# Optimization experiments

Measured on AMD Instinct MI355X. Metric: run time of the kernel, lower is better.

Reference implementation:

```python
import jax, jax.numpy as jnp
import numpy as np

WX, WY = 32, 32
N = WX * WY                      # 1024 tokens
TOKEN_DIM = 1024
QKV = 512
H = 8
HD = QKV // H                    # 64
TOPK = 32
B = 64
NUM_UNIQUE = (2 * WX - 1) * (2 * WY - 1)  # 3969 unique relative offsets
LN_EPS = 1e-5


def _make_rel_idx():
    # identical to torch create_positional_biases: lexicographic unique index of (dx, dy)
    ix = np.arange(N) // WY
    iy = np.arange(N) % WY
    dx = ix[:, None] - ix[None, :]
    dy = iy[:, None] - iy[None, :]
    rel = (dx + WX - 1) * (2 * WY - 1) + (dy + WY - 1)
    return jnp.asarray(rel, dtype=jnp.int32)  # [N, N]


def _layernorm(x, g, b):
    m = jnp.mean(x, axis=-1, keepdims=True)
    v = jnp.mean(jnp.square(x - m), axis=-1, keepdims=True)
    return (x - m) * jax.lax.rsqrt(v + LN_EPS) * g + b


def setup_inputs() -> dict:
    key = jax.random.key(0)
    ks = jax.random.split(key, 12)
    s = 0.02
    return {
        "x": jax.random.normal(ks[0], (B, N, TOKEN_DIM), jnp.float32),
        "scorer_w": jax.random.normal(ks[1], (1, TOKEN_DIM), jnp.float32) * s,
        "scorer_b": jnp.zeros((1,), jnp.float32),
        "ln_g": jnp.ones((TOKEN_DIM,), jnp.float32),
        "ln_b": jnp.zeros((TOKEN_DIM,), jnp.float32),
        "qk_w": jax.random.normal(ks[2], (QKV, TOKEN_DIM), jnp.float32) * s,
        "qk_b": jnp.zeros((QKV,), jnp.float32),
        "v_w": jax.random.normal(ks[3], (QKV, TOKEN_DIM), jnp.float32) * s,
        "v_b": jnp.zeros((QKV,), jnp.float32),
        "skip_w": jax.random.normal(ks[4], (QKV, TOKEN_DIM), jnp.float32) * s,
        "skip_b": jnp.zeros((QKV,), jnp.float32),
        "out_w": jax.random.normal(ks[5], (QKV, QKV), jnp.float32) * s,
        "out_b": jnp.zeros((QKV,), jnp.float32),
        "fc_w": jax.random.normal(ks[6], (2, QKV), jnp.float32) * s,
        "fc_b": jnp.zeros((2,), jnp.float32),
        "unique_bias": jax.random.normal(ks[7], (NUM_UNIQUE,), jnp.float32) * s,
        "rel_idx": _make_rel_idx(),
    }


def reference(x, scorer_w, scorer_b, ln_g, ln_b, qk_w, qk_b, v_w, v_b,
              skip_w, skip_b, out_w, out_b, fc_w, fc_b, unique_bias, rel_idx):
    # token selection (eval path: argmax of relevance logits)
    logits = jnp.einsum('bnd,od->bno', x, scorer_w)[..., 0] + scorer_b[0]  # [B, N]
    sel_idx = jnp.argmax(logits, axis=-1)                                   # [B]
    sel_tok = x[jnp.arange(B), sel_idx]                                     # [B, D]

    x_n = _layernorm(x, ln_g, ln_b)
    s_n = _layernorm(sel_tok, ln_g, ln_b)

    value = (jnp.einsum('bnd,qd->bnq', x_n, v_w) + v_b).reshape(B, N, H, HD).transpose(0, 2, 1, 3)  # [B,H,N,hd]
    key_t = (jnp.einsum('bnd,qd->bnq', x_n, qk_w) + qk_b).reshape(B, N, H, HD).transpose(0, 2, 1, 3)
    query = (s_n @ qk_w.T + qk_b).reshape(B, H, HD)                         # [B,H,hd]

    attn = jnp.einsum('bhd,bhnd->bhn', query, key_t) / jnp.sqrt(jnp.float32(HD))  # [B,H,N]
    bias = unique_bias[rel_idx[sel_idx]]                                    # gather: [B, N]
    attn = jax.nn.softmax(attn + bias[:, None, :], axis=-1)

    # top-k sparsification + renormalization
    _, topk_idx = jax.lax.top_k(attn, TOPK)                                 # [B,H,K]
    mask = jax.nn.one_hot(topk_idx, N, dtype=attn.dtype).sum(axis=-2)       # [B,H,N] 0/1
    attn = attn * mask
    attn = attn / (attn.sum(axis=-1, keepdims=True) + 1e-9)

    y = jnp.einsum('bhn,bhnd->bhd', attn, value).reshape(B, QKV)            # [B, QKV]
    skip = sel_tok @ skip_w.T + skip_b
    y = jax.nn.relu(y + skip)
    # dropout is identity in eval mode
    y = y @ out_w.T + out_b
    y = y @ fc_w.T + fc_b
    return y  # [B, 2]
```

## Files before the change

### kernel.cpp

```cpp
#include <hip/hip_runtime.h>
#include <hip/hip_bf16.h>
#include <math.h>

#define WX 32
#define WY 32
#define NTOK 1024
#define TD 1024
#define QKV 512
#define NH 8
#define HD 64
#define TOPK 32
#define BB 64

__device__ __forceinline__ float wred_sum(float v){
  #pragma unroll
  for (int o=32;o;o>>=1) v += __shfl_xor(v,o,64);
  return v;
}
__device__ __forceinline__ float wred_max(float v){
  #pragma unroll
  for (int o=32;o;o>>=1) v = fmaxf(v, __shfl_xor(v,o,64));
  return v;
}
__device__ __forceinline__ float dot4f(float4 a, float4 b){
  return a.x*b.x + a.y*b.y + a.z*b.z + a.w*b.w;
}

__global__ __launch_bounds__(256) void k1_stats(
    const float* __restrict__ x, const float* __restrict__ sw, const float* __restrict__ sb,
    float* __restrict__ mean, float* __restrict__ rstd, float* __restrict__ logit){
  int wave = threadIdx.x >> 6, lane = threadIdx.x & 63;
  int tok = blockIdx.x*4 + wave;
  const float4* xp = (const float4*)(x + (size_t)tok*TD);
  const float4* sp = (const float4*)sw;
  float s1=0.f, s2=0.f, sd=0.f;
  #pragma unroll
  for (int j=0;j<4;j++){
    float4 v = xp[lane + j*64];
    float4 w = sp[lane + j*64];
    s1 += v.x+v.y+v.z+v.w;
    s2 += v.x*v.x + v.y*v.y + v.z*v.z + v.w*v.w;
    sd += dot4f(v,w);
  }
  s1 = wred_sum(s1); s2 = wred_sum(s2); sd = wred_sum(sd);
  if (lane==0){
    float m = s1*(1.f/1024.f);
    float var = s2*(1.f/1024.f) - m*m;
    mean[tok] = m;
    rstd[tok] = rsqrtf(var + 1e-5f);
    logit[tok] = sd + sb[0];
  }
}

__global__ __launch_bounds__(256) void k2_prep(
    const float* __restrict__ x, const float* __restrict__ logit,
    const float* __restrict__ mean, const float* __restrict__ rstd,
    const float* __restrict__ lng, const float* __restrict__ lnb,
    const float* __restrict__ qkw, const float* __restrict__ qkb,
    int* __restrict__ selI, float* __restrict__ gu8,
    float* __restrict__ Aw, float* __restrict__ C0w){
  __shared__ float sn[TD];
  __shared__ float qs[QKV];
  __shared__ float redV[4]; __shared__ int redI[4];
  __shared__ float red16[64];
  __shared__ int sel_s;
  int b = blockIdx.x, t = threadIdx.x, lane = t&63, wave = t>>6;

  const float* lg = logit + b*NTOK;
  float bv = -INFINITY; int bi = 0;
  #pragma unroll
  for (int j=0;j<4;j++){ int idx = t*4+j; float v = lg[idx]; if (v > bv){ bv=v; bi=idx; } }
  #pragma unroll
  for (int o=32;o;o>>=1){
    float vv = __shfl_xor(bv,o,64); int ii = __shfl_xor(bi,o,64);
    if (vv > bv || (vv == bv && ii < bi)){ bv=vv; bi=ii; }
  }
  if (lane==0){ redV[wave]=bv; redI[wave]=bi; }
  __syncthreads();
  if (t==0){
    float v = redV[0]; int i = redI[0];
    for (int w=1; w<4; w++){ if (redV[w] > v || (redV[w]==v && redI[w]<i)){ v=redV[w]; i=redI[w]; } }
    sel_s = i; selI[b] = i;
  }
  __syncthreads();
  int sel = sel_s;
  float m = mean[b*NTOK+sel], r = rstd[b*NTOK+sel];
  float4 g4 = ((const float4*)lng)[t];
  float4 b4 = ((const float4*)lnb)[t];
  {
    float4 xv = ((const float4*)(x + ((size_t)b*NTOK + sel)*TD))[t];
    float4 s4;
    s4.x = (xv.x-m)*r*g4.x + b4.x;
    s4.y = (xv.y-m)*r*g4.y + b4.y;
    s4.z = (xv.z-m)*r*g4.z + b4.z;
    s4.w = (xv.w-m)*r*g4.w + b4.w;
    ((float4*)sn)[t] = s4;
  }
  __syncthreads();
  #pragma unroll
  for (int rr=0; rr<2; rr++){
    int j = t + rr*256;
    const float4* wr = (const float4*)(qkw + (size_t)j*TD);
    float acc = 0.f;
    for (int d=0; d<256; d++) acc += dot4f(wr[d], ((const float4*)sn)[d]);
    qs[j] = acc + qkb[j];
  }
  __syncthreads();
  float su[NH], bu[NH];
  #pragma unroll
  for (int h=0; h<NH; h++){
    float4 acc = make_float4(0.f,0.f,0.f,0.f);
    for (int c=0; c<HD; c++){
      float qv = qs[h*HD+c];
      float4 w = ((const float4*)(qkw + (size_t)(h*HD+c)*TD))[t];
      acc.x += qv*w.x; acc.y += qv*w.y; acc.z += qv*w.z; acc.w += qv*w.w;
    }
    su[h] = g4.x*acc.x + g4.y*acc.y + g4.z*acc.z + g4.w*acc.w;
    bu[h] = b4.x*acc.x + b4.y*acc.y + b4.z*acc.z + b4.w*acc.w;
    float4 gu;
    gu.x = acc.x*g4.x*0.125f; gu.y = acc.y*g4.y*0.125f;
    gu.z = acc.z*g4.z*0.125f; gu.w = acc.w*g4.w*0.125f;
    ((float4*)(gu8 + ((size_t)b*NH + h)*TD))[t] = gu;
  }
  #pragma unroll
  for (int h=0; h<NH; h++){ su[h] = wred_sum(su[h]); bu[h] = wred_sum(bu[h]); }
  if (lane==0){
    #pragma unroll
    for (int h=0; h<NH; h++){ red16[wave*16+h] = su[h]; red16[wave*16+8+h] = bu[h]; }
  }
  __syncthreads();
  if (t < NH){
    int h = t;
    float s = 0.f, bb = 0.f;
    for (int w=0; w<4; w++){ s += red16[w*16+h]; bb += red16[w*16+8+h]; }
    float qb = 0.f;
    for (int c=0; c<HD; c++) qb += qs[h*HD+c]*qkb[h*HD+c];
    Aw[b*NH+h] = s*0.125f;
    C0w[b*NH+h] = (bb + qb)*0.125f;
  }
}

__global__ __launch_bounds__(128) void k3_attn(
    const float* __restrict__ x, const float* __restrict__ mean, const float* __restrict__ rstd,
    const float* __restrict__ gu8, const float* __restrict__ Aw, const float* __restrict__ C0w,
    const int* __restrict__ selI, const int* __restrict__ relIdx, const float* __restrict__ ub,
    float* __restrict__ attL){
  int b = blockIdx.x >> 3;
  int n = (blockIdx.x & 7)*128 + threadIdx.x;
  int tok = b*NTOK + n;
  float m = mean[tok], r = rstd[tok];
  int sel = selI[b];
  float bias = ub[relIdx[sel*NTOK + n]];
  const float4* xp = (const float4*)(x + (size_t)tok*TD);
  const float4* gp = (const float4*)(gu8 + (size_t)b*NH*TD);
  float4 acc[NH];
  #pragma unroll
  for (int h=0; h<NH; h++) acc[h] = make_float4(0.f,0.f,0.f,0.f);
  for (int d0=0; d0<256; d0+=4){
    #pragma unroll
    for (int jj=0; jj<4; jj++){
      float4 xv = xp[d0+jj];
      #pragma unroll
      for (int h=0; h<NH; h++){
        float4 g = gp[h*256 + d0 + jj];
        acc[h].x += xv.x*g.x; acc[h].y += xv.y*g.y;
        acc[h].z += xv.z*g.z; acc[h].w += xv.w*g.w;
      }
    }
  }
  #pragma unroll
  for (int h=0; h<NH; h++){
    float s = acc[h].x + acc[h].y + acc[h].z + acc[h].w;
    float L = r*s - r*m*Aw[b*NH+h] + C0w[b*NH+h] + bias;
    attL[((size_t)b*NH + h)*NTOK + n] = L;
  }
}

__global__ __launch_bounds__(256) void k4_topkv(
    const float* __restrict__ x, const float* __restrict__ mean, const float* __restrict__ rstd,
    const float* __restrict__ lng, const float* __restrict__ lnb,
    const float* __restrict__ vw, const float* __restrict__ vb,
    const float* __restrict__ attL, float* __restrict__ yout){
  __shared__ float candV[4]; __shared__ int candI[4];
  __shared__ float redf[4];
  __shared__ float selV[TOPK]; __shared__ int selIs[TOPK];
  __shared__ float aa[TOPK]; __shared__ float am[TOPK];
  __shared__ float xbar[TD];
  __shared__ float red2[256];
  int b = blockIdx.x >> 3, h = blockIdx.x & 7;
  int t = threadIdx.x, lane = t&63, wave = t>>6;

  float4 Lv = ((const float4*)(attL + ((size_t)b*NH + h)*NTOK))[t];
  float lm = fmaxf(fmaxf(Lv.x,Lv.y), fmaxf(Lv.z,Lv.w));
  lm = wred_max(lm);
  if (lane==0) redf[wave] = lm;
  __syncthreads();
  float maxL = fmaxf(fmaxf(redf[0],redf[1]), fmaxf(redf[2],redf[3]));
  __syncthreads();
  float ev[4];
  ev[0] = __expf(Lv.x - maxL); ev[1] = __expf(Lv.y - maxL);
  ev[2] = __expf(Lv.z - maxL); ev[3] = __expf(Lv.w - maxL);
  float zp = ev[0]+ev[1]+ev[2]+ev[3];
  zp = wred_sum(zp);
  if (lane==0) redf[wave] = zp;
  __syncthreads();
  float Z = redf[0]+redf[1]+redf[2]+redf[3];
  __syncthreads();

  float S = 0.f;
  for (int k=0; k<TOPK; k++){
    float bv = -1.f; int bi = 1<<20;
    #pragma unroll
    for (int j=0;j<4;j++){ if (ev[j] > bv){ bv = ev[j]; bi = t*4+j; } }
    #pragma unroll
    for (int o=32;o;o>>=1){
      float vv = __shfl_xor(bv,o,64); int ii = __shfl_xor(bi,o,64);
      if (vv > bv || (vv == bv && ii < bi)){ bv=vv; bi=ii; }
    }
    if (lane==0){ candV[wave]=bv; candI[wave]=bi; }
    __syncthreads();
    float wv = candV[0]; int wi = candI[0];
    #pragma unroll
    for (int w=1; w<4; w++){
      float vv = candV[w]; int ii = candI[w];
      if (vv > wv || (vv == wv && ii < wi)){ wv=vv; wi=ii; }
    }
    if ((wi>>2) == t) ev[wi&3] = -1.f;
    if (t==0){ selV[k]=wv; selIs[k]=wi; }
    S += wv;
    __syncthreads();
  }

  float denom = S + 1e-9f*Z;
  float W = S/denom;
  if (t < TOPK){
    int ni = selIs[t];
    float w = selV[t]/denom;
    float a = w * rstd[b*NTOK+ni];
    aa[t] = a; am[t] = a*mean[b*NTOK+ni];
  }
  __syncthreads();
  float c = 0.f;
  #pragma unroll
  for (int k=0;k<TOPK;k++) c += am[k];

  float4 acc = make_float4(0.f,0.f,0.f,0.f);
  for (int k=0;k<TOPK;k++){
    float a = aa[k];
    float4 xv = ((const float4*)(x + ((size_t)b*NTOK + selIs[k])*TD))[t];
    acc.x += a*xv.x; acc.y += a*xv.y; acc.z += a*xv.z; acc.w += a*xv.w;
  }
  float4 g4 = ((const float4*)lng)[t];
  float4 b4 = ((const float4*)lnb)[t];
  float4 xb;
  xb.x = g4.x*(acc.x - c) + b4.x*W;
  xb.y = g4.y*(acc.y - c) + b4.y*W;
  xb.z = g4.z*(acc.z - c) + b4.z*W;
  xb.w = g4.w*(acc.w - c) + b4.w*W;
  ((float4*)xbar)[t] = xb;
  __syncthreads();

  int co = t >> 2, part = t & 3;
  const float4* vp = (const float4*)(vw + (size_t)(h*HD+co)*TD + part*256);
  const float4* xp2 = ((const float4*)xbar) + part*64;
  float a2 = 0.f;
  for (int j=0;j<64;j++) a2 += dot4f(vp[j], xp2[j]);
  red2[t] = a2;
  __syncthreads();
  if (part==0){
    float y = red2[t] + red2[t+1] + red2[t+2] + red2[t+3] + vb[h*HD+co]*W;
    yout[b*QKV + h*HD + co] = y;
  }
}

__global__ __launch_bounds__(256) void k5_epi(
    const float* __restrict__ x, const int* __restrict__ selI,
    const float* __restrict__ skw, const float* __restrict__ skb,
    const float* __restrict__ ow, const float* __restrict__ ob,
    const float* __restrict__ fcw, const float* __restrict__ fcb,
    const float* __restrict__ yv, float* __restrict__ out){
  __shared__ float xs[TD];
  __shared__ float t1[QKV];
  __shared__ float t2[QKV];
  __shared__ float redA[4]; __shared__ float redB[4];
  int b = blockIdx.x, t = threadIdx.x, lane = t&63, wave = t>>6;
  int sel = selI[b];
  ((float4*)xs)[t] = ((const float4*)(x + ((size_t)b*NTOK + sel)*TD))[t];
  __syncthreads();
  #pragma unroll
  for (int rr=0; rr<2; rr++){
    int j = t + rr*256;
    const float4* wr = (const float4*)(skw + (size_t)j*TD);
    float acc = 0.f;
    for (int d=0; d<256; d++) acc += dot4f(wr[d], ((const float4*)xs)[d]);
    t1[j] = fmaxf(yv[b*QKV + j] + acc + skb[j], 0.f);
  }
  __syncthreads();
  #pragma unroll
  for (int rr=0; rr<2; rr++){
    int j = t + rr*256;
    const float4* wr = (const float4*)(ow + (size_t)j*QKV);
    float acc = 0.f;
    for (int d=0; d<128; d++) acc += dot4f(wr[d], ((const float4*)t1)[d]);
    t2[j] = acc + ob[j];
  }
  __syncthreads();
  float a0 = 0.f, a1 = 0.f;
  #pragma unroll
  for (int rr=0; rr<2; rr++){
    int d = t + rr*256;
    float v = t2[d];
    a0 += v*fcw[d]; a1 += v*fcw[QKV+d];
  }
  a0 = wred_sum(a0); a1 = wred_sum(a1);
  if (lane==0){ redA[wave]=a0; redB[wave]=a1; }
  __syncthreads();
  if (t==0){
    out[b*2+0] = redA[0]+redA[1]+redA[2]+redA[3] + fcb[0];
    out[b*2+1] = redB[0]+redB[1]+redB[2]+redB[3] + fcb[1];
  }
}

extern "C" void kernel_launch(void* const* d_in, const int* in_sizes, int n_in,
                              void* d_out, int out_size, void* d_ws, size_t ws_size,
                              hipStream_t stream) {
  const float* x   = (const float*)d_in[0];
  const float* sw  = (const float*)d_in[1];
  const float* sb  = (const float*)d_in[2];
  const float* lng = (const float*)d_in[3];
  const float* lnb = (const float*)d_in[4];
  const float* qkw = (const float*)d_in[5];
  const float* qkb = (const float*)d_in[6];
  const float* vw  = (const float*)d_in[7];
  const float* vb  = (const float*)d_in[8];
  const float* skw = (const float*)d_in[9];
  const float* skb = (const float*)d_in[10];
  const float* ow  = (const float*)d_in[11];
  const float* ob  = (const float*)d_in[12];
  const float* fcw = (const float*)d_in[13];
  const float* fcb = (const float*)d_in[14];
  const float* ub  = (const float*)d_in[15];
  const int*   ri  = (const int*)d_in[16];
  float* out = (float*)d_out;

  float* wsf   = (float*)d_ws;
  float* logit = wsf;
  float* mean  = wsf + 65536;
  float* rstd  = wsf + 131072;
  int*   selI  = (int*)(wsf + 196608);
  float* gu8   = wsf + 196672;
  float* Aw    = wsf + 720960;
  float* C0w   = wsf + 721472;
  float* attL  = wsf + 721984;
  float* yv    = wsf + 1246272;

  k1_stats<<<16384, 256, 0, stream>>>(x, sw, sb, mean, rstd, logit);
  k2_prep<<<BB, 256, 0, stream>>>(x, logit, mean, rstd, lng, lnb, qkw, qkb,
                                  selI, gu8, Aw, C0w);
  k3_attn<<<BB*8, 128, 0, stream>>>(x, mean, rstd, gu8, Aw, C0w, selI, ri, ub, attL);
  k4_topkv<<<BB*NH, 256, 0, stream>>>(x, mean, rstd, lng, lnb, vw, vb, attL, yv);
  k5_epi<<<BB, 256, 0, stream>>>(x, selI, skw, skb, ow, ob, fcw, fcb, yv, out);
}
```

Baseline: 680.9 us.

## Parallelize prep, attention, top-k and epilogue kernels across more blocks

Splits the per-batch prep kernel across heads (B*H blocks) and precomputes the relative-position bias once per batch. Rewrites the attention-logit kernel so each wave handles a token, with gu vectors held in registers, coalesced x loads with prefetch, and wave reductions. Replaces the serial block-wide top-k with per-wave top-32 lists merged by one thread, and splits the epilogue into three wider-grid kernels with split-K dot products. This targets underutilized low-block-count kernels and uncoalesced per-thread x row reads, at the cost of redundant argmax/layernorm work per head and extra launches.

```diff
diff --git a/kernel.cpp b/kernel.cpp
--- a/kernel.cpp
+++ b/kernel.cpp
@@ -57,14 +57,16 @@
     const float* __restrict__ mean, const float* __restrict__ rstd,
     const float* __restrict__ lng, const float* __restrict__ lnb,
     const float* __restrict__ qkw, const float* __restrict__ qkb,
+    const int* __restrict__ relIdx, const float* __restrict__ ub,
     int* __restrict__ selI, float* __restrict__ gu8,
-    float* __restrict__ Aw, float* __restrict__ C0w){
+    float* __restrict__ Aw, float* __restrict__ C0w, float* __restrict__ biasArr){
   __shared__ float sn[TD];
-  __shared__ float qs[QKV];
+  __shared__ float qs[HD];
+  __shared__ float red[256];
   __shared__ float redV[4]; __shared__ int redI[4];
-  __shared__ float red16[64];
   __shared__ int sel_s;
-  int b = blockIdx.x, t = threadIdx.x, lane = t&63, wave = t>>6;
+  int b = blockIdx.x >> 3, h = blockIdx.x & 7;
+  int t = threadIdx.x, lane = t&63, wave = t>>6;
 
   const float* lg = logit + b*NTOK;
   float bv = -INFINITY; int bi = 0;
@@ -80,7 +82,8 @@
   if (t==0){
     float v = redV[0]; int i = redI[0];
     for (int w=1; w<4; w++){ if (redV[w] > v || (redV[w]==v && redI[w]<i)){ v=redV[w]; i=redI[w]; } }
-    sel_s = i; selI[b] = i;
+    sel_s = i;
+    if (h==0) selI[b] = i;
   }
   __syncthreads();
   int sel = sel_s;
@@ -97,82 +100,108 @@
     ((float4*)sn)[t] = s4;
   }
   __syncthreads();
-  #pragma unroll
-  for (int rr=0; rr<2; rr++){
-    int j = t + rr*256;
-    const float4* wr = (const float4*)(qkw + (size_t)j*TD);
+  {
+    int row = t>>2, part = t&3;
+    const float4* wr = (const float4*)(qkw + (size_t)(h*HD+row)*TD + part*256);
+    const float4* xp = ((const float4*)sn) + part*64;
     float acc = 0.f;
-    for (int d=0; d<256; d++) acc += dot4f(wr[d], ((const float4*)sn)[d]);
-    qs[j] = acc + qkb[j];
-  }
-  __syncthreads();
-  float su[NH], bu[NH];
-  #pragma unroll
-  for (int h=0; h<NH; h++){
-    float4 acc = make_float4(0.f,0.f,0.f,0.f);
-    for (int c=0; c<HD; c++){
-      float qv = qs[h*HD+c];
-      float4 w = ((const float4*)(qkw + (size_t)(h*HD+c)*TD))[t];
-      acc.x += qv*w.x; acc.y += qv*w.y; acc.z += qv*w.z; acc.w += qv*w.w;
-    }
-    su[h] = g4.x*acc.x + g4.y*acc.y + g4.z*acc.z + g4.w*acc.w;
-    bu[h] = b4.x*acc.x + b4.y*acc.y + b4.z*acc.z + b4.w*acc.w;
+    #pragma unroll 8
+    for (int j=0;j<64;j++) acc += dot4f(wr[j], xp[j]);
+    red[t] = acc;
+  }
+  __syncthreads();
+  if (t < HD) qs[t] = red[t*4]+red[t*4+1]+red[t*4+2]+red[t*4+3] + qkb[h*HD+t];
+  __syncthreads();
+  float4 acc = make_float4(0.f,0.f,0.f,0.f);
+  for (int c=0;c<HD;c++){
+    float qv = qs[c];
+    float4 w = ((const float4*)(qkw + (size_t)(h*HD+c)*TD))[t];
+    acc.x += qv*w.x; acc.y += qv*w.y; acc.z += qv*w.z; acc.w += qv*w.w;
+  }
+  {
     float4 gu;
     gu.x = acc.x*g4.x*0.125f; gu.y = acc.y*g4.y*0.125f;
     gu.z = acc.z*g4.z*0.125f; gu.w = acc.w*g4.w*0.125f;
-    ((float4*)(gu8 + ((size_t)b*NH + h)*TD))[t] = gu;
-  }
-  #pragma unroll
-  for (int h=0; h<NH; h++){ su[h] = wred_sum(su[h]); bu[h] = wred_sum(bu[h]); }
-  if (lane==0){
-    #pragma unroll
-    for (int h=0; h<NH; h++){ red16[wave*16+h] = su[h]; red16[wave*16+8+h] = bu[h]; }
-  }
-  __syncthreads();
-  if (t < NH){
-    int h = t;
-    float s = 0.f, bb = 0.f;
-    for (int w=0; w<4; w++){ s += red16[w*16+h]; bb += red16[w*16+8+h]; }
-    float qb = 0.f;
-    for (int c=0; c<HD; c++) qb += qs[h*HD+c]*qkb[h*HD+c];
-    Aw[b*NH+h] = s*0.125f;
-    C0w[b*NH+h] = (bb + qb)*0.125f;
-  }
-}
-
-__global__ __launch_bounds__(128) void k3_attn(
+    ((float4*)(gu8 + ((size_t)(b*NH+h))*TD))[t] = gu;
+  }
+  float su_p = g4.x*acc.x + g4.y*acc.y + g4.z*acc.z + g4.w*acc.w;
+  float bu_p = b4.x*acc.x + b4.y*acc.y + b4.z*acc.z + b4.w*acc.w;
+  su_p = wred_sum(su_p); bu_p = wred_sum(bu_p);
+  if (lane==0){ red[wave] = su_p; red[8+wave] = bu_p; }
+  if (wave==0){
+    float qb_p = qs[lane]*qkb[h*HD+lane];
+    qb_p = wred_sum(qb_p);
+    if (lane==0) red[16] = qb_p;
+  }
+  __syncthreads();
+  if (t==0){
+    float s  = red[0]+red[1]+red[2]+red[3];
+    float bb = red[8]+red[9]+red[10]+red[11];
+    Aw[b*NH+h]  = s*0.125f;
+    C0w[b*NH+h] = (bb + red[16])*0.125f;
+  }
+  if (h==0){
+    const int* rp = relIdx + (size_t)sel*NTOK;
+    #pragma unroll
+    for (int j=0;j<4;j++){
+      int n = t*4+j;
+      biasArr[b*NTOK+n] = ub[rp[n]];
+    }
+  }
+}
+
+__global__ __launch_bounds__(256) void k3_attn(
     const float* __restrict__ x, const float* __restrict__ mean, const float* __restrict__ rstd,
     const float* __restrict__ gu8, const float* __restrict__ Aw, const float* __restrict__ C0w,
-    const int* __restrict__ selI, const int* __restrict__ relIdx, const float* __restrict__ ub,
-    float* __restrict__ attL){
-  int b = blockIdx.x >> 3;
-  int n = (blockIdx.x & 7)*128 + threadIdx.x;
-  int tok = b*NTOK + n;
-  float m = mean[tok], r = rstd[tok];
-  int sel = selI[b];
-  float bias = ub[relIdx[sel*NTOK + n]];
-  const float4* xp = (const float4*)(x + (size_t)tok*TD);
+    const float* __restrict__ biasArr, float* __restrict__ attL){
+  int b = blockIdx.x >> 4;
+  int chunk = blockIdx.x & 15;
+  int lane = threadIdx.x & 63, wave = threadIdx.x >> 6;
+
   const float4* gp = (const float4*)(gu8 + (size_t)b*NH*TD);
-  float4 acc[NH];
-  #pragma unroll
-  for (int h=0; h<NH; h++) acc[h] = make_float4(0.f,0.f,0.f,0.f);
-  for (int d0=0; d0<256; d0+=4){
-    #pragma unroll
-    for (int jj=0; jj<4; jj++){
-      float4 xv = xp[d0+jj];
+  float4 G[NH][4];
+  #pragma unroll
+  for (int h=0;h<NH;h++)
+    #pragma unroll
+    for (int j=0;j<4;j++)
+      G[h][j] = gp[h*256 + j*64 + lane];
+  float Ah[NH], Ch[NH];
+  #pragma unroll
+  for (int h=0;h<NH;h++){ Ah[h] = Aw[b*NH+h]; Ch[h] = C0w[b*NH+h]; }
+
+  const int base = chunk*64 + wave*16;
+  float4 cur[4];
+  {
+    const float4* xp = (const float4*)(x + ((size_t)b*NTOK + base)*TD);
+    #pragma unroll
+    for (int j=0;j<4;j++) cur[j] = xp[j*64 + lane];
+  }
+  for (int i=0;i<16;i++){
+    int n = base + i;
+    int tok = b*NTOK + n;
+    float4 nxt[4];
+    if (i < 15){
+      const float4* xp = (const float4*)(x + (size_t)(tok+1)*TD);
       #pragma unroll
-      for (int h=0; h<NH; h++){
-        float4 g = gp[h*256 + d0 + jj];
-        acc[h].x += xv.x*g.x; acc[h].y += xv.y*g.y;
-        acc[h].z += xv.z*g.z; acc[h].w += xv.w*g.w;
-      }
-    }
-  }
-  #pragma unroll
-  for (int h=0; h<NH; h++){
-    float s = acc[h].x + acc[h].y + acc[h].z + acc[h].w;
-    float L = r*s - r*m*Aw[b*NH+h] + C0w[b*NH+h] + bias;
-    attL[((size_t)b*NH + h)*NTOK + n] = L;
+      for (int j=0;j<4;j++) nxt[j] = xp[j*64 + lane];
+    }
+    float m = mean[tok], r = rstd[tok], bias = biasArr[b*NTOK+n];
+    float s[NH];
+    #pragma unroll
+    for (int h=0;h<NH;h++){
+      float a = dot4f(cur[0],G[h][0]) + dot4f(cur[1],G[h][1])
+              + dot4f(cur[2],G[h][2]) + dot4f(cur[3],G[h][3]);
+      s[h] = wred_sum(a);
+    }
+    #pragma unroll
+    for (int h=0;h<NH;h++){
+      if (lane == h)
+        attL[((size_t)b*NH+h)*NTOK + n] = r*s[h] - r*m*Ah[h] + Ch[h] + bias;
+    }
+    if (i < 15){
+      #pragma unroll
+      for (int j=0;j<4;j++) cur[j] = nxt[j];
+    }
   }
 }
 
@@ -181,9 +210,10 @@
     const float* __restrict__ lng, const float* __restrict__ lnb,
     const float* __restrict__ vw, const float* __restrict__ vb,
     const float* __restrict__ attL, float* __restrict__ yout){
-  __shared__ float candV[4]; __shared__ int candI[4];
   __shared__ float redf[4];
+  __shared__ float wtopV[4][TOPK]; __shared__ int wtopI[4][TOPK];
   __shared__ float selV[TOPK]; __shared__ int selIs[TOPK];
+  __shared__ float Ssh;
   __shared__ float aa[TOPK]; __shared__ float am[TOPK];
   __shared__ float xbar[TD];
   __shared__ float red2[256];
@@ -205,10 +235,8 @@
   if (lane==0) redf[wave] = zp;
   __syncthreads();
   float Z = redf[0]+redf[1]+redf[2]+redf[3];
-  __syncthreads();
-
-  float S = 0.f;
-  for (int k=0; k<TOPK; k++){
+
+  for (int k=0;k<TOPK;k++){
     float bv = -1.f; int bi = 1<<20;
     #pragma unroll
     for (int j=0;j<4;j++){ if (ev[j] > bv){ bv = ev[j]; bi = t*4+j; } }
@@ -217,20 +245,31 @@
       float vv = __shfl_xor(bv,o,64); int ii = __shfl_xor(bi,o,64);
       if (vv > bv || (vv == bv && ii < bi)){ bv=vv; bi=ii; }
     }
-    if (lane==0){ candV[wave]=bv; candI[wave]=bi; }
-    __syncthreads();
-    float wv = candV[0]; int wi = candI[0];
-    #pragma unroll
-    for (int w=1; w<4; w++){
-      float vv = candV[w]; int ii = candI[w];
-      if (vv > wv || (vv == wv && ii < wi)){ wv=vv; wi=ii; }
-    }
-    if ((wi>>2) == t) ev[wi&3] = -1.f;
-    if (t==0){ selV[k]=wv; selIs[k]=wi; }
-    S += wv;
-    __syncthreads();
-  }
-
+    #pragma unroll
+    for (int j=0;j<4;j++){ if (bi == t*4+j) ev[j] = -1.f; }
+    if (lane==0){ wtopV[wave][k] = bv; wtopI[wave][k] = bi; }
+  }
+  __syncthreads();
+  if (t==0){
+    int p0=0,p1=0,p2=0,p3=0;
+    float S = 0.f;
+    for (int k=0;k<TOPK;k++){
+      float bv = -1.f; int bi = 1<<20, bw = 0;
+      float v; int ii;
+      v = wtopV[0][p0]; ii = wtopI[0][p0]; if (v > bv || (v==bv && ii<bi)){ bv=v; bi=ii; bw=0; }
+      v = wtopV[1][p1]; ii = wtopI[1][p1]; if (v > bv || (v==bv && ii<bi)){ bv=v; bi=ii; bw=1; }
+      v = wtopV[2][p2]; ii = wtopI[2][p2]; if (v > bv || (v==bv && ii<bi)){ bv=v; bi=ii; bw=2; }
+      v = wtopV[3][p3]; ii = wtopI[3][p3]; if (v > bv || (v==bv && ii<bi)){ bv=v; bi=ii; bw=3; }
+      if (bw==0) p0 = (p0<TOPK-1)?p0+1:p0;
+      else if (bw==1) p1 = (p1<TOPK-1)?p1+1:p1;
+      else if (bw==2) p2 = (p2<TOPK-1)?p2+1:p2;
+      else p3 = (p3<TOPK-1)?p3+1:p3;
+      selV[k] = bv; selIs[k] = bi; S += bv;
+    }
+    Ssh = S;
+  }
+  __syncthreads();
+  float S = Ssh;
   float denom = S + 1e-9f*Z;
   float W = S/denom;
   if (t < TOPK){
@@ -264,6 +303,7 @@
   const float4* vp = (const float4*)(vw + (size_t)(h*HD+co)*TD + part*256);
   const float4* xp2 = ((const float4*)xbar) + part*64;
   float a2 = 0.f;
+  #pragma unroll 8
   for (int j=0;j<64;j++) a2 += dot4f(vp[j], xp2[j]);
   red2[t] = a2;
   __syncthreads();
@@ -273,52 +313,65 @@
   }
 }
 
-__global__ __launch_bounds__(256) void k5_epi(
+__global__ __launch_bounds__(256) void k5a(
     const float* __restrict__ x, const int* __restrict__ selI,
     const float* __restrict__ skw, const float* __restrict__ skb,
-    const float* __restrict__ ow, const float* __restrict__ ob,
-    const float* __restrict__ fcw, const float* __restrict__ fcb,
-    const float* __restrict__ yv, float* __restrict__ out){
+    const float* __restrict__ yv, float* __restrict__ t1ws){
   __shared__ float xs[TD];
-  __shared__ float t1[QKV];
-  __shared__ float t2[QKV];
-  __shared__ float redA[4]; __shared__ float redB[4];
-  int b = blockIdx.x, t = threadIdx.x, lane = t&63, wave = t>>6;
+  __shared__ float red[256];
+  int b = blockIdx.x >> 3, chunk = blockIdx.x & 7;
+  int t = threadIdx.x;
   int sel = selI[b];
   ((float4*)xs)[t] = ((const float4*)(x + ((size_t)b*NTOK + sel)*TD))[t];
   __syncthreads();
-  #pragma unroll
-  for (int rr=0; rr<2; rr++){
-    int j = t + rr*256;
-    const float4* wr = (const float4*)(skw + (size_t)j*TD);
-    float acc = 0.f;
-    for (int d=0; d<256; d++) acc += dot4f(wr[d], ((const float4*)xs)[d]);
-    t1[j] = fmaxf(yv[b*QKV + j] + acc + skb[j], 0.f);
-  }
-  __syncthreads();
-  #pragma unroll
-  for (int rr=0; rr<2; rr++){
-    int j = t + rr*256;
-    const float4* wr = (const float4*)(ow + (size_t)j*QKV);
-    float acc = 0.f;
-    for (int d=0; d<128; d++) acc += dot4f(wr[d], ((const float4*)t1)[d]);
-    t2[j] = acc + ob[j];
-  }
-  __syncthreads();
+  int row = chunk*64 + (t>>2), part = t&3;
+  const float4* wr = (const float4*)(skw + (size_t)row*TD + part*256);
+  const float4* xp = ((const float4*)xs) + part*64;
+  float acc = 0.f;
+  #pragma unroll 8
+  for (int j=0;j<64;j++) acc += dot4f(wr[j], xp[j]);
+  red[t] = acc;
+  __syncthreads();
+  if (part==0){
+    float v = red[t]+red[t+1]+red[t+2]+red[t+3];
+    t1ws[b*QKV+row] = fmaxf(yv[b*QKV+row] + v + skb[row], 0.f);
+  }
+}
+
+__global__ __launch_bounds__(256) void k5b(
+    const float* __restrict__ t1ws, const float* __restrict__ ow,
+    const float* __restrict__ ob, float* __restrict__ t2ws){
+  __shared__ float ts[QKV];
+  __shared__ float red[256];
+  int b = blockIdx.x >> 3, chunk = blockIdx.x & 7;
+  int t = threadIdx.x;
+  if (t < 128) ((float4*)ts)[t] = ((const float4*)(t1ws + (size_t)b*QKV))[t];
+  __syncthreads();
+  int row = chunk*64 + (t>>2), part = t&3;
+  const float4* wr = (const float4*)(ow + (size_t)row*QKV + part*128);
+  const float4* xp = ((const float4*)ts) + part*32;
+  float acc = 0.f;
+  #pragma unroll
+  for (int j=0;j<32;j++) acc += dot4f(wr[j], xp[j]);
+  red[t] = acc;
+  __syncthreads();
+  if (part==0)
+    t2ws[b*QKV+row] = red[t]+red[t+1]+red[t+2]+red[t+3] + ob[row];
+}
+
+__global__ __launch_bounds__(64) void k5c(
+    const float* __restrict__ t2ws, const float* __restrict__ fcw,
+    const float* __restrict__ fcb, float* __restrict__ out){
+  int b = blockIdx.x, lane = threadIdx.x;
   float a0 = 0.f, a1 = 0.f;
   #pragma unroll
-  for (int rr=0; rr<2; rr++){
-    int d = t + rr*256;
-    float v = t2[d];
+  for (int j=0;j<8;j++){
+    int d = j*64 + lane;
+    float v = t2ws[(size_t)b*QKV + d];
     a0 += v*fcw[d]; a1 += v*fcw[QKV+d];
   }
   a0 = wred_sum(a0); a1 = wred_sum(a1);
-  if (lane==0){ redA[wave]=a0; redB[wave]=a1; }
-  __syncthreads();
-  if (t==0){
-    out[b*2+0] = redA[0]+redA[1]+redA[2]+redA[3] + fcb[0];
-    out[b*2+1] = redB[0]+redB[1]+redB[2]+redB[3] + fcb[1];
-  }
+  if (lane==0){ out[b*2+0] = a0 + fcb[0]; out[b*2+1] = a1 + fcb[1]; }
 }
 
 extern "C" void kernel_launch(void* const* d_in, const int* in_sizes, int n_in,
@@ -343,21 +396,26 @@
   const int*   ri  = (const int*)d_in[16];
   float* out = (float*)d_out;
 
-  float* wsf   = (float*)d_ws;
-  float* logit = wsf;
-  float* mean  = wsf + 65536;
-  float* rstd  = wsf + 131072;
-  int*   selI  = (int*)(wsf + 196608);
-  float* gu8   = wsf + 196672;
-  float* Aw    = wsf + 720960;
-  float* C0w   = wsf + 721472;
-  float* attL  = wsf + 721984;
-  float* yv    = wsf + 1246272;
+  float* wsf     = (float*)d_ws;
+  float* logit   = wsf;
+  float* mean    = wsf + 65536;
+  float* rstd    = wsf + 131072;
+  int*   selI    = (int*)(wsf + 196608);
+  float* gu8     = wsf + 196672;
+  float* Aw      = wsf + 720960;
+  float* C0w     = wsf + 721472;
+  float* biasArr = wsf + 721984;
+  float* attL    = wsf + 787520;
+  float* yv      = wsf + 1311808;
+  float* t1ws    = wsf + 1344576;
+  float* t2ws    = wsf + 1377344;
 
   k1_stats<<<16384, 256, 0, stream>>>(x, sw, sb, mean, rstd, logit);
-  k2_prep<<<BB, 256, 0, stream>>>(x, logit, mean, rstd, lng, lnb, qkw, qkb,
-                                  selI, gu8, Aw, C0w);
-  k3_attn<<<BB*8, 128, 0, stream>>>(x, mean, rstd, gu8, Aw, C0w, selI, ri, ub, attL);
+  k2_prep<<<BB*NH, 256, 0, stream>>>(x, logit, mean, rstd, lng, lnb, qkw, qkb,
+                                     ri, ub, selI, gu8, Aw, C0w, biasArr);
+  k3_attn<<<BB*16, 256, 0, stream>>>(x, mean, rstd, gu8, Aw, C0w, biasArr, attL);
   k4_topkv<<<BB*NH, 256, 0, stream>>>(x, mean, rstd, lng, lnb, vw, vb, attL, yv);
-  k5_epi<<<BB, 256, 0, stream>>>(x, selI, skw, skb, ow, ob, fcw, fcb, yv, out);
-}
+  k5a<<<BB*8, 256, 0, stream>>>(x, selI, skw, skb, yv, t1ws);
+  k5b<<<BB*8, 256, 0, stream>>>(t1ws, ow, ob, t2ws);
+  k5c<<<BB, 64, 0, stream>>>(t2ws, fcw, fcb, out);
+}
```

Result: faster. 557.0 us (-18.2%).
